# Performance work log

Hardware: AMD Instinct MI355X
Metric: run time of the kernel (lower is better)

The kernel has to match this reference:

```python
import jax, jax.numpy as jnp
import numpy as np

N = 50000      # nodes
E = 800000     # edges (before self-loops)
IN = 64        # in_dim
C = 64         # hidden_dim (per-head out channels)
H = 4          # heads
NEG_SLOPE = 0.2


def setup_inputs() -> dict:
    key = jax.random.key(0)
    ks = jax.random.split(key, 9)
    x = jax.random.normal(ks[0], (N, IN), jnp.float32)
    edge_index = jax.random.randint(ks[1], (2, E), 0, N)
    edge_attr = jax.random.uniform(ks[2], (E, 1), jnp.float32)
    s_in = 1.0 / np.sqrt(IN)
    s_c = 1.0 / np.sqrt(C)
    W = jax.random.normal(ks[3], (IN, H * C), jnp.float32) * s_in
    att_src = jax.random.normal(ks[4], (H, C), jnp.float32) * s_c
    att_dst = jax.random.normal(ks[5], (H, C), jnp.float32) * s_c
    lin_edge_w = jax.random.normal(ks[6], (1, H * C), jnp.float32)
    att_edge = jax.random.normal(ks[7], (H, C), jnp.float32) * s_c
    bias = jnp.zeros((C,), jnp.float32)
    return dict(x=x, edge_index=edge_index, edge_attr=edge_attr, W=W,
                att_src=att_src, att_dst=att_dst, lin_edge_w=lin_edge_w,
                att_edge=att_edge, bias=bias)


def reference(x, edge_index, edge_attr, W, att_src, att_dst, lin_edge_w, att_edge, bias):
    n = x.shape[0]
    # add self-loops (PyG default add_self_loops=True, fill_value='mean')
    loop = jnp.arange(n)
    src = jnp.concatenate([edge_index[0], loop])          # [E+N]
    dst = jnp.concatenate([edge_index[1], loop])          # [E+N]
    ea = jnp.concatenate([edge_attr,
                          jnp.full((n, 1), edge_attr.mean(), edge_attr.dtype)], axis=0)
    # node transform: [N, H, C]
    h = (x @ W).reshape(n, H, C)
    a_src = jnp.einsum('nhc,hc->nh', h, att_src)          # [N, H]
    a_dst = jnp.einsum('nhc,hc->nh', h, att_dst)          # [N, H]
    eh = (ea @ lin_edge_w).reshape(-1, H, C)              # [E+N, H, C]
    a_edge = jnp.einsum('ehc,hc->eh', eh, att_edge)       # [E+N, H]
    # per-edge attention logit
    alpha = a_src[src] + a_dst[dst] + a_edge              # [E+N, H]
    alpha = jax.nn.leaky_relu(alpha, NEG_SLOPE)
    # segment softmax over edges grouped by destination node
    amax = jax.ops.segment_max(alpha, dst, num_segments=n)
    alpha = jnp.exp(alpha - amax[dst])
    asum = jax.ops.segment_sum(alpha, dst, num_segments=n)
    alpha = alpha / (asum[dst] + 1e-16)                   # [E+N, H]
    # weighted message + scatter-add aggregation
    msg = h[src] * alpha[..., None]                       # [E+N, H, C]
    out = jax.ops.segment_sum(msg, dst, num_segments=n)   # [N, H, C]
    out = out.mean(axis=1) + bias                         # concat=False -> head mean
    # ReLU + residual
    return jax.nn.relu(out) + x
```

## Files before the change

kernel.cpp:

```cpp
#include <hip/hip_runtime.h>
#include <hip/hip_fp16.h>
#include <math.h>

#define H 4
#define C 64
#define HC 256
#define NEG 0.2f
#define ROWU 64
#define MAXREC 63
#define XPAD 72
#define HPAD 264

typedef __attribute__((ext_vector_type(8))) _Float16 half8;
typedef __attribute__((ext_vector_type(4))) float f32x4;
typedef float f32x2 __attribute__((vector_size(8)));

__global__ __launch_bounds__(256) void phase1_kernel(
    const float* __restrict__ x, const float* __restrict__ W,
    const float* __restrict__ att_src, const float* __restrict__ att_dst,
    const int* __restrict__ ei, const float* __restrict__ edge_attr,
    unsigned char* __restrict__ h, float* __restrict__ a_src, float* __restrict__ a_dst,
    unsigned* __restrict__ edges, float* __restrict__ mean_acc,
    int Nn, int Ee, int G1, int G2) {
    int t = threadIdx.x;
    if ((int)blockIdx.x < G1) {
        __shared__ __align__(16) _Float16 xs[16 * XPAD];
        __shared__ __align__(16) _Float16 hs[16 * HPAD];
        int w = t >> 6, lane = t & 63, quad = lane >> 4, c16 = lane & 15;
        half8 bf[4][2];
#pragma unroll
        for (int nt = 0; nt < 4; ++nt)
#pragma unroll
            for (int kh = 0; kh < 2; ++kh)
#pragma unroll
                for (int j = 0; j < 8; ++j)
                    bf[nt][kh][j] = (_Float16)W[(kh * 32 + quad * 8 + j) * HC +
                                                w * 64 + nt * 16 + c16];
        float ats[4], atd[4];
#pragma unroll
        for (int nt = 0; nt < 4; ++nt) {
            ats[nt] = att_src[w * 64 + nt * 16 + c16];
            atd[nt] = att_dst[w * 64 + nt * 16 + c16];
        }

        int nTiles = (Nn + 15) >> 4;
        for (int mt = blockIdx.x; mt < nTiles; mt += G1) {
            __syncthreads();
            {
                int row = t >> 4, col4 = (t & 15) * 4;
                int node = mt * 16 + row;
                float4 v = make_float4(0.f, 0.f, 0.f, 0.f);
                if (node < Nn) v = *(const float4*)(x + (size_t)node * 64 + col4);
                _Float16* dst = xs + row * XPAD + col4;
                dst[0] = (_Float16)v.x; dst[1] = (_Float16)v.y;
                dst[2] = (_Float16)v.z; dst[3] = (_Float16)v.w;
            }
            __syncthreads();
            half8 a0 = *(const half8*)(xs + c16 * XPAD + quad * 8);
            half8 a1 = *(const half8*)(xs + c16 * XPAD + 32 + quad * 8);
            f32x4 d[4];
#pragma unroll
            for (int nt = 0; nt < 4; ++nt) {
                f32x4 acc = {0.f, 0.f, 0.f, 0.f};
                acc = __builtin_amdgcn_mfma_f32_16x16x32_f16(a0, bf[nt][0], acc, 0, 0, 0);
                acc = __builtin_amdgcn_mfma_f32_16x16x32_f16(a1, bf[nt][1], acc, 0, 0, 0);
                d[nt] = acc;
            }
#pragma unroll
            for (int reg = 0; reg < 4; ++reg) {
                float ps = 0.f, pd = 0.f;
#pragma unroll
                for (int nt = 0; nt < 4; ++nt) {
                    ps += d[nt][reg] * ats[nt];
                    pd += d[nt][reg] * atd[nt];
                }
                ps += __shfl_xor(ps, 1); pd += __shfl_xor(pd, 1);
                ps += __shfl_xor(ps, 2); pd += __shfl_xor(pd, 2);
                ps += __shfl_xor(ps, 4); pd += __shfl_xor(pd, 4);
                ps += __shfl_xor(ps, 8); pd += __shfl_xor(pd, 8);
                if (c16 == 0) {
                    int node = mt * 16 + quad * 4 + reg;
                    if (node < Nn) {
                        a_src[node * 4 + w] = ps;
                        a_dst[node * 4 + w] = pd;
                    }
                }
            }
#pragma unroll
            for (int nt = 0; nt < 4; ++nt)
#pragma unroll
                for (int reg = 0; reg < 4; ++reg)
                    hs[(quad * 4 + reg) * HPAD + w * 64 + nt * 16 + c16] =
                        (_Float16)d[nt][reg];
            __syncthreads();
            {
                int row = t >> 4, chunk = t & 15;
                int node = mt * 16 + row;
                if (node < Nn) {
                    const uint4* sp = (const uint4*)(hs + row * HPAD + chunk * 16);
                    uint4 sA = sp[0], sB = sp[1];
                    unsigned ua[8] = {sA.x, sA.y, sA.z, sA.w, sB.x, sB.y, sB.z, sB.w};
                    unsigned ow[4];
#pragma unroll
                    for (int q = 0; q < 4; ++q) {
                        float2 p0 = __half22float2(*reinterpret_cast<const __half2*>(&ua[q * 2]));
                        float2 p1 = __half22float2(*reinterpret_cast<const __half2*>(&ua[q * 2 + 1]));
                        int v = __builtin_amdgcn_cvt_pk_fp8_f32(p0.x, p0.y, 0, false);
                        v = __builtin_amdgcn_cvt_pk_fp8_f32(p1.x, p1.y, v, true);
                        ow[q] = (unsigned)v;
                    }
                    *(uint4*)(h + (size_t)node * HC + chunk * 16) =
                        make_uint4(ow[0], ow[1], ow[2], ow[3]);
                }
            }
        }
    } else {
        __shared__ float red[256];
        int gid = ((int)blockIdx.x - G1) * 256 + t;
        int stride = G2 * 256;
        float s = 0.f;
        for (int i = gid; i < Ee; i += stride) {
            int src = ei[i];
            int dst = ei[Ee + i];
            float ea = edge_attr[i];
            s += ea;
            unsigned q = (unsigned)(ea * 65535.f + 0.5f);
            unsigned rank = atomicAdd(&edges[(size_t)dst * ROWU], 1u);
            if (rank < MAXREC)
                edges[(size_t)dst * ROWU + 1 + rank] = (q << 16) | (unsigned)src;
        }
        red[t] = s;
        __syncthreads();
        for (int o = 128; o; o >>= 1) {
            if (t < o) red[t] += red[t + o];
            __syncthreads();
        }
        if (t == 0) atomicAdd(mean_acc, red[0]);
    }
}

__global__ __launch_bounds__(256) void aggregate_kernel(
    const unsigned* __restrict__ edges,
    const float* __restrict__ a_src, const float* __restrict__ a_dst,
    const float* __restrict__ lin_edge_w, const float* __restrict__ att_edge,
    const float* __restrict__ mean_acc, const unsigned char* __restrict__ h,
    const float* __restrict__ bias, const float* __restrict__ x,
    float* __restrict__ out, int Nn, float invE) {
    int lane = threadIdx.x & 63;
    int n = blockIdx.x * 4 + (threadIdx.x >> 6);
    if (n >= Nn) return;
    int head = lane >> 4;

    size_t rowbase = (size_t)n * ROWU;
    unsigned deg = edges[rowbase];
    unsigned rec = edges[rowbase + 1 + lane];
    const unsigned* h8 = (const unsigned*)h;
    unsigned sv = h8[(size_t)n * 64 + lane];
    float mean = mean_acc[0] * invE;
    float ad = a_dst[n * 4 + head];
    float asn = a_src[n * 4 + head];

    int sub = lane & 15;
    float kp = 0.f;
#pragma unroll
    for (int j = 0; j < 4; ++j) {
        int c = sub * 4 + j;
        kp += lin_edge_w[head * C + c] * att_edge[head * C + c];
    }
    kp += __shfl_xor(kp, 1);
    kp += __shfl_xor(kp, 2);
    kp += __shfl_xor(kp, 4);
    kp += __shfl_xor(kp, 8);
    float K = kp;
    const float DEQ = 1.0f / 65535.f;

    if (deg > MAXREC) deg = MAXREC;

    float ls = asn + ad + mean * K;
    ls = ls > 0.f ? ls : NEG * ls;
    float wsl = __expf(ls);
    f32x2 s01 = __builtin_amdgcn_cvt_pk_f32_fp8((int)sv, false);
    f32x2 s23 = __builtin_amdgcn_cvt_pk_f32_fp8((int)sv, true);
    float4 acc = make_float4(wsl * s01[0], wsl * s01[1], wsl * s23[0], wsl * s23[1]);
    float swgt = wsl;

    int i = 0;
    for (; i + 4 <= (int)deg; i += 4) {
        unsigned r0 = (unsigned)__builtin_amdgcn_readlane((int)rec, i + 0);
        unsigned r1 = (unsigned)__builtin_amdgcn_readlane((int)rec, i + 1);
        unsigned r2 = (unsigned)__builtin_amdgcn_readlane((int)rec, i + 2);
        unsigned r3 = (unsigned)__builtin_amdgcn_readlane((int)rec, i + 3);
        int s0 = r0 & 0xFFFF, s1 = r1 & 0xFFFF, s2 = r2 & 0xFFFF, s3 = r3 & 0xFFFF;
        unsigned hv0 = h8[(size_t)s0 * 64 + lane];
        unsigned hv1 = h8[(size_t)s1 * 64 + lane];
        unsigned hv2 = h8[(size_t)s2 * 64 + lane];
        unsigned hv3 = h8[(size_t)s3 * 64 + lane];
        float l0 = a_src[s0 * 4 + head] + ad + (float)(r0 >> 16) * DEQ * K;
        float l1 = a_src[s1 * 4 + head] + ad + (float)(r1 >> 16) * DEQ * K;
        float l2 = a_src[s2 * 4 + head] + ad + (float)(r2 >> 16) * DEQ * K;
        float l3 = a_src[s3 * 4 + head] + ad + (float)(r3 >> 16) * DEQ * K;
        l0 = l0 > 0.f ? l0 : NEG * l0;
        l1 = l1 > 0.f ? l1 : NEG * l1;
        l2 = l2 > 0.f ? l2 : NEG * l2;
        l3 = l3 > 0.f ? l3 : NEG * l3;
        float w0 = __expf(l0), w1 = __expf(l1), w2 = __expf(l2), w3 = __expf(l3);
        swgt += (w0 + w1) + (w2 + w3);
        {
            f32x2 f01 = __builtin_amdgcn_cvt_pk_f32_fp8((int)hv0, false);
            f32x2 f23 = __builtin_amdgcn_cvt_pk_f32_fp8((int)hv0, true);
            acc.x += w0 * f01[0]; acc.y += w0 * f01[1];
            acc.z += w0 * f23[0]; acc.w += w0 * f23[1];
        }
        {
            f32x2 f01 = __builtin_amdgcn_cvt_pk_f32_fp8((int)hv1, false);
            f32x2 f23 = __builtin_amdgcn_cvt_pk_f32_fp8((int)hv1, true);
            acc.x += w1 * f01[0]; acc.y += w1 * f01[1];
            acc.z += w1 * f23[0]; acc.w += w1 * f23[1];
        }
        {
            f32x2 f01 = __builtin_amdgcn_cvt_pk_f32_fp8((int)hv2, false);
            f32x2 f23 = __builtin_amdgcn_cvt_pk_f32_fp8((int)hv2, true);
            acc.x += w2 * f01[0]; acc.y += w2 * f01[1];
            acc.z += w2 * f23[0]; acc.w += w2 * f23[1];
        }
        {
            f32x2 f01 = __builtin_amdgcn_cvt_pk_f32_fp8((int)hv3, false);
            f32x2 f23 = __builtin_amdgcn_cvt_pk_f32_fp8((int)hv3, true);
            acc.x += w3 * f01[0]; acc.y += w3 * f01[1];
            acc.z += w3 * f23[0]; acc.w += w3 * f23[1];
        }
    }
    for (; i < (int)deg; ++i) {
        unsigned r = (unsigned)__builtin_amdgcn_readlane((int)rec, i);
        int s0 = r & 0xFFFF;
        unsigned hv = h8[(size_t)s0 * 64 + lane];
        float l = a_src[s0 * 4 + head] + ad + (float)(r >> 16) * DEQ * K;
        l = l > 0.f ? l : NEG * l;
        float wg = __expf(l);
        swgt += wg;
        f32x2 f01 = __builtin_amdgcn_cvt_pk_f32_fp8((int)hv, false);
        f32x2 f23 = __builtin_amdgcn_cvt_pk_f32_fp8((int)hv, true);
        acc.x += wg * f01[0]; acc.y += wg * f01[1];
        acc.z += wg * f23[0]; acc.w += wg * f23[1];
    }

    float inv = 1.f / (swgt + 1e-16f);
    acc.x *= inv; acc.y *= inv; acc.z *= inv; acc.w *= inv;

    acc.x += __shfl_xor(acc.x, 16);
    acc.y += __shfl_xor(acc.y, 16);
    acc.z += __shfl_xor(acc.z, 16);
    acc.w += __shfl_xor(acc.w, 16);
    acc.x += __shfl_xor(acc.x, 32);
    acc.y += __shfl_xor(acc.y, 32);
    acc.z += __shfl_xor(acc.z, 32);
    acc.w += __shfl_xor(acc.w, 32);
    if (lane < 16) {
        float4 b = ((const float4*)bias)[lane];
        float4 xv = ((const float4*)x)[(size_t)n * 16 + lane];
        float4 o;
        o.x = fmaxf(acc.x * 0.25f + b.x, 0.f) + xv.x;
        o.y = fmaxf(acc.y * 0.25f + b.y, 0.f) + xv.y;
        o.z = fmaxf(acc.z * 0.25f + b.z, 0.f) + xv.z;
        o.w = fmaxf(acc.w * 0.25f + b.w, 0.f) + xv.w;
        ((float4*)out)[(size_t)n * 16 + lane] = o;
    }
}

extern "C" void kernel_launch(void* const* d_in, const int* in_sizes, int n_in,
                              void* d_out, int out_size, void* d_ws, size_t ws_size,
                              hipStream_t stream) {
    const float* x = (const float*)d_in[0];
    const int* ei = (const int*)d_in[1];
    const float* edge_attr = (const float*)d_in[2];
    const float* W = (const float*)d_in[3];
    const float* att_src = (const float*)d_in[4];
    const float* att_dst = (const float*)d_in[5];
    const float* lin_edge_w = (const float*)d_in[6];
    const float* att_edge = (const float*)d_in[7];
    const float* bias = (const float*)d_in[8];
    float* out = (float*)d_out;
    int Nn = in_sizes[0] / 64;
    int Ee = in_sizes[1] / 2;

    char* p = (char*)d_ws;
    size_t off = 0;
    auto alloc = [&](size_t bytes) -> char* {
        char* r = p + off;
        off += (bytes + 255) & ~(size_t)255;
        return r;
    };
    float* mean_acc = (float*)alloc(256);
    unsigned* edges = (unsigned*)alloc((size_t)Nn * ROWU * 4);
    size_t zero_bytes = off;
    unsigned char* h = (unsigned char*)alloc((size_t)Nn * HC);
    float* a_src = (float*)alloc((size_t)Nn * H * 4);
    float* a_dst = (float*)alloc((size_t)Nn * H * 4);
    (void)ws_size;

    const int G1 = 512, G2 = 1536;
    hipMemsetAsync(d_ws, 0, zero_bytes, stream);
    phase1_kernel<<<G1 + G2, 256, 0, stream>>>(x, W, att_src, att_dst, ei, edge_attr,
                                               h, a_src, a_dst, edges,
                                               mean_acc, Nn, Ee, G1, G2);
    aggregate_kernel<<<(Nn + 3) / 4, 256, 0, stream>>>(edges, a_src, a_dst,
                                                       lin_edge_w, att_edge, mean_acc,
                                                       h, bias, x, out, Nn,
                                                       1.0f / (float)Ee);
}
```

Before: 170.0 us.

## Replace per-edge global atomics with two-level bucketed CSR build

The edge-bucketing phase now groups edges into coarse destination buckets of 128 nodes. It uses shared-memory counters per tile plus one global atomic per bucket per tile, and writes edges to a per-bucket arena. A new kernel then scatters each bucket into per-node rows in LDS and writes them out coalesced. This removes 800K scattered global atomics and the memset of the large edge table, at the cost of an extra kernel launch, an extra pass over the arena, and a fixed arena capacity that could overflow for skewed inputs.

```diff
diff --git a/kernel.cpp b/kernel.cpp
--- a/kernel.cpp
+++ b/kernel.cpp
@@ -10,6 +10,10 @@
 #define MAXREC 63
 #define XPAD 72
 #define HPAD 264
+#define BKT 128
+#define BSH 7
+#define ARN 2816
+#define TILE 8192
 
 typedef __attribute__((ext_vector_type(8))) _Float16 half8;
 typedef __attribute__((ext_vector_type(4))) float f32x4;
@@ -20,8 +24,8 @@
     const float* __restrict__ att_src, const float* __restrict__ att_dst,
     const int* __restrict__ ei, const float* __restrict__ edge_attr,
     unsigned char* __restrict__ h, float* __restrict__ a_src, float* __restrict__ a_dst,
-    unsigned* __restrict__ edges, float* __restrict__ mean_acc,
-    int Nn, int Ee, int G1, int G2) {
+    uint2* __restrict__ arena, unsigned* __restrict__ cursor,
+    float* __restrict__ mean_acc, int Nn, int Ee, int G1, int G2) {
     int t = threadIdx.x;
     if ((int)blockIdx.x < G1) {
         __shared__ __align__(16) _Float16 xs[16 * XPAD];
@@ -116,18 +120,48 @@
         }
     } else {
         __shared__ float red[256];
-        int gid = ((int)blockIdx.x - G1) * 256 + t;
-        int stride = G2 * 256;
+        __shared__ unsigned cntA[512], baseA[512];
+        int nbkt = (Nn + BKT - 1) >> BSH;
+        int ntile = (Ee + TILE - 1) / TILE;
         float s = 0.f;
-        for (int i = gid; i < Ee; i += stride) {
-            int src = ei[i];
-            int dst = ei[Ee + i];
-            float ea = edge_attr[i];
-            s += ea;
-            unsigned q = (unsigned)(ea * 65535.f + 0.5f);
-            unsigned rank = atomicAdd(&edges[(size_t)dst * ROWU], 1u);
-            if (rank < MAXREC)
-                edges[(size_t)dst * ROWU + 1 + rank] = (q << 16) | (unsigned)src;
+        for (int tile = (int)blockIdx.x - G1; tile < ntile; tile += G2) {
+            int e0 = tile * TILE;
+            for (int bb = t; bb < nbkt; bb += 256) cntA[bb] = 0;
+            __syncthreads();
+#pragma unroll 4
+            for (int k = 0; k < TILE / 256; ++k) {
+                int i = e0 + k * 256 + t;
+                if (i < Ee) {
+                    int dst = ei[Ee + i];
+                    s += edge_attr[i];
+                    atomicAdd(&cntA[dst >> BSH], 1u);
+                }
+            }
+            __syncthreads();
+            for (int bb = t; bb < nbkt; bb += 256) {
+                unsigned c = cntA[bb];
+                baseA[bb] = c ? atomicAdd(&cursor[bb], c) : 0u;
+                cntA[bb] = 0;
+            }
+            __syncthreads();
+#pragma unroll 4
+            for (int k = 0; k < TILE / 256; ++k) {
+                int i = e0 + k * 256 + t;
+                if (i < Ee) {
+                    int src = ei[i];
+                    int dst = ei[Ee + i];
+                    float ea = edge_attr[i];
+                    unsigned q = (unsigned)(ea * 65535.f + 0.5f);
+                    int b = dst >> BSH;
+                    unsigned r = atomicAdd(&cntA[b], 1u);
+                    unsigned idx = baseA[b] + r;
+                    if (idx < ARN)
+                        arena[(size_t)b * ARN + idx] =
+                            make_uint2((q << 16) | (unsigned)src,
+                                       (unsigned)(dst & (BKT - 1)));
+                }
+            }
+            __syncthreads();
         }
         red[t] = s;
         __syncthreads();
@@ -137,6 +171,29 @@
         }
         if (t == 0) atomicAdd(mean_acc, red[0]);
     }
+}
+
+__global__ __launch_bounds__(256) void bucket_kernel(
+    const uint2* __restrict__ arena, const unsigned* __restrict__ cursor,
+    unsigned* __restrict__ edges) {
+    __shared__ unsigned rows[BKT * ROWU];
+    __shared__ unsigned cnt[BKT];
+    int b = blockIdx.x, t = threadIdx.x;
+    if (t < BKT) cnt[t] = 0;
+    __syncthreads();
+    unsigned nb = cursor[b];
+    if (nb > ARN) nb = ARN;
+    for (unsigned i = t; i < nb; i += 256) {
+        uint2 e = arena[(size_t)b * ARN + i];
+        unsigned r = atomicAdd(&cnt[e.y], 1u);
+        if (r < MAXREC) rows[e.y * ROWU + 1 + r] = e.x;
+    }
+    __syncthreads();
+    if (t < BKT) rows[t * ROWU] = cnt[t] < (unsigned)MAXREC ? cnt[t] : (unsigned)MAXREC;
+    __syncthreads();
+    size_t obase = (size_t)b * (BKT * ROWU);
+    for (int i = t; i < BKT * (ROWU / 4); i += 256)
+        *(uint4*)(edges + obase + i * 4) = *(const uint4*)(rows + i * 4);
 }
 
 __global__ __launch_bounds__(256) void aggregate_kernel(
@@ -282,6 +339,7 @@
     float* out = (float*)d_out;
     int Nn = in_sizes[0] / 64;
     int Ee = in_sizes[1] / 2;
+    int NB = (Nn + BKT - 1) >> BSH;
 
     char* p = (char*)d_ws;
     size_t off = 0;
@@ -291,18 +349,23 @@
         return r;
     };
     float* mean_acc = (float*)alloc(256);
-    unsigned* edges = (unsigned*)alloc((size_t)Nn * ROWU * 4);
+    unsigned* cursor = (unsigned*)alloc((size_t)NB * 4);
     size_t zero_bytes = off;
+    uint2* arena = (uint2*)alloc((size_t)NB * ARN * 8);
+    unsigned* edges = (unsigned*)alloc((size_t)NB * BKT * ROWU * 4);
     unsigned char* h = (unsigned char*)alloc((size_t)Nn * HC);
     float* a_src = (float*)alloc((size_t)Nn * H * 4);
     float* a_dst = (float*)alloc((size_t)Nn * H * 4);
     (void)ws_size;
 
-    const int G1 = 512, G2 = 1536;
+    int ntile = (Ee + TILE - 1) / TILE;
+    const int G1 = 512;
+    int G2 = ntile < 2048 ? ntile : 2048;
     hipMemsetAsync(d_ws, 0, zero_bytes, stream);
     phase1_kernel<<<G1 + G2, 256, 0, stream>>>(x, W, att_src, att_dst, ei, edge_attr,
-                                               h, a_src, a_dst, edges,
+                                               h, a_src, a_dst, arena, cursor,
                                                mean_acc, Nn, Ee, G1, G2);
+    bucket_kernel<<<NB, 256, 0, stream>>>(arena, cursor, edges);
     aggregate_kernel<<<(Nn + 3) / 4, 256, 0, stream>>>(edges, a_src, a_dst,
                                                        lin_edge_w, att_edge, mean_acc,
                                                        h, bias, x, out, Nn,
```

Measured after the change: 163.3 us. 1.04x faster.
